# Kernel optimization log

Measured on AMD Instinct MI355X. Metric: run time of the kernel, lower is better.

The kernel has to match this reference:

```python
import jax, jax.numpy as jnp
import numpy as np

N = 100000   # nodes
E = 3200000  # edges (avg degree 32)
IN = 128     # in_channels
H = 128      # hidden_channels
G = 512      # graphs in batch


def setup_inputs() -> dict:
    key = jax.random.key(0)
    ks = jax.random.split(key, 8)
    x = jax.random.normal(ks[0], (N, IN), dtype=jnp.float32)
    edge_index = jax.random.randint(ks[1], (2, E), 0, N, dtype=jnp.int64)
    batch = jnp.sort(jax.random.randint(ks[2], (N,), 0, G, dtype=jnp.int64))
    s_in = 1.0 / np.sqrt(IN)
    s_h = 1.0 / np.sqrt(H)
    W1 = jax.random.normal(ks[3], (IN, H), dtype=jnp.float32) * s_in
    b1 = jnp.zeros((H,), dtype=jnp.float32)
    W2 = jax.random.normal(ks[4], (H, H), dtype=jnp.float32) * s_h
    b2 = jnp.zeros((H,), dtype=jnp.float32)
    Wc = jax.random.normal(ks[5], (H, 1), dtype=jnp.float32) * s_h
    bc = jnp.zeros((1,), dtype=jnp.float32)
    return {"x": x, "edge_index": edge_index, "batch": batch,
            "W1": W1, "b1": b1, "W2": W2, "b2": b2, "Wc": Wc, "bc": bc}


def _gcn_conv(x, W, b, src, dst, n):
    # PyG GCNConv: x' = D^{-1/2} (A+I) D^{-1/2} X W + b  (self-loops already in src/dst)
    h = x @ W                                      # [n, H] small GEMM
    ones = jnp.ones(src.shape[0], dtype=h.dtype)
    deg = jax.ops.segment_sum(ones, dst, num_segments=n)
    dinv = jnp.where(deg > 0, jax.lax.rsqrt(deg), 0.0)
    norm = dinv[src] * dinv[dst]                   # [E+n]
    msgs = h[src] * norm[:, None]                  # gather + scale (memory-bound)
    return jax.ops.segment_sum(msgs, dst, num_segments=n) + b


def reference(x, edge_index, batch, W1, b1, W2, b2, Wc, bc):
    n = x.shape[0]
    loop = jnp.arange(n, dtype=edge_index.dtype)
    src = jnp.concatenate([edge_index[0], loop])   # add self-loops
    dst = jnp.concatenate([edge_index[1], loop])
    h = jax.nn.relu(_gcn_conv(x, W1, b1, src, dst, n))
    h = jax.nn.relu(_gcn_conv(h, W2, b2, src, dst, n))
    # global_mean_pool: segment mean over graph ids
    counts = jax.ops.segment_sum(jnp.ones(n, dtype=h.dtype), batch, num_segments=G)
    sums = jax.ops.segment_sum(h, batch, num_segments=G)
    pooled = sums / jnp.maximum(counts, 1.0)[:, None]   # [G, H]
    return jax.nn.sigmoid(pooled @ Wc + bc)             # [G, 1]
```

## Files before the change

### kernel.cpp

```cpp
#include <hip/hip_runtime.h>

typedef unsigned short ushort_t;
typedef unsigned int uint_t;
typedef unsigned char u8_t;

typedef __bf16 bf16x8 __attribute__((ext_vector_type(8)));
typedef float f32x4 __attribute__((ext_vector_type(4)));
typedef uint_t uint32x4 __attribute__((ext_vector_type(4)));
typedef uint_t uint32x2 __attribute__((ext_vector_type(2)));
typedef _Float16 h2 __attribute__((ext_vector_type(2)));

#define EPB 16384
#define NSH 7
#define CAP 6144

__device__ __forceinline__ float b2f(ushort_t u) {
    union { uint_t ui; float f; } c; c.ui = ((uint_t)u) << 16; return c.f;
}
__device__ __forceinline__ ushort_t f2b(float f) {
    union { float f; uint_t ui; } c; c.f = f;
    uint_t u = c.ui;
    uint_t r = (u + 0x7fffu + ((u >> 16) & 1u)) >> 16;
    return (ushort_t)r;
}
__device__ __forceinline__ u8_t f2e5(float x) {
    ushort_t h = __builtin_bit_cast(ushort_t, (_Float16)x);
    uint_t r = ((uint_t)h + 0x7Fu + ((h >> 8) & 1u)) >> 8;
    return (u8_t)r;
}
__device__ __forceinline__ void upk_add(uint_t d, h2* acc) {
    uint_t A = __builtin_amdgcn_perm(0u, d, 0x010C000Cu);
    uint_t B = __builtin_amdgcn_perm(0u, d, 0x030C020Cu);
    acc[0] += __builtin_bit_cast(h2, A);
    acc[1] += __builtin_bit_cast(h2, B);
}

__global__ __launch_bounds__(256) void p1_hist(const int* __restrict__ dst,
                                               int* __restrict__ H,
                                               const float* __restrict__ W1,
                                               const float* __restrict__ W2,
                                               ushort_t* __restrict__ W1t,
                                               ushort_t* __restrict__ W2t,
                                               int E, int NBLK, int B) {
    int t = threadIdx.x, c = blockIdx.x;
    if (c >= NBLK) {
        int idx = (c - NBLK) * 256 + t;
        int sel = idx >> 14;
        int i = idx & 16383;
        int k = i >> 7, nn = i & 127;
        const float* S = sel ? W2 : W1;
        ushort_t* D = sel ? W2t : W1t;
        D[nn * 128 + k] = f2b(S[k * 128 + nn]);
        return;
    }
    __shared__ int hist[1024];
    for (int b = t; b < 1024; b += 256) hist[b] = 0;
    __syncthreads();
    int base = c * EPB;
    int lim = min(E - base, EPB);
    for (int i = t; i < lim; i += 256)
        atomicAdd(&hist[dst[base + i] >> NSH], 1);
    __syncthreads();
    for (int b = t; b < B; b += 256) H[b * NBLK + c] = hist[b];
}

__global__ __launch_bounds__(256) void reduce256(const int* __restrict__ in,
                                                 int* __restrict__ bsums, int n) {
    __shared__ int s[256];
    int t = threadIdx.x, g = blockIdx.x * 256 + t;
    s[t] = (g < n) ? in[g] : 0;
    __syncthreads();
    for (int o = 128; o > 0; o >>= 1) {
        if (t < o) s[t] += s[t + o];
        __syncthreads();
    }
    if (t == 0) bsums[blockIdx.x] = s[0];
}

__global__ __launch_bounds__(512) void scan_small(const int* __restrict__ in,
                                                  int* __restrict__ outEx, int n) {
    __shared__ int s[512];
    int t = threadIdx.x;
    int v = (t < n) ? in[t] : 0;
    s[t] = v;
    __syncthreads();
    for (int o = 1; o < 512; o <<= 1) {
        int x = 0;
        if (t >= o) x = s[t - o];
        __syncthreads();
        s[t] += x;
        __syncthreads();
    }
    if (t < n) outEx[t] = s[t] - v;
}

__global__ __launch_bounds__(256) void scan256ex(const int* __restrict__ in,
                                                 const int* __restrict__ boffs,
                                                 int* __restrict__ outEx, int n) {
    __shared__ int s[256];
    int t = threadIdx.x, g = blockIdx.x * 256 + t;
    int v = (g < n) ? in[g] : 0;
    s[t] = v;
    __syncthreads();
    for (int o = 1; o < 256; o <<= 1) {
        int x = 0;
        if (t >= o) x = s[t - o];
        __syncthreads();
        s[t] += x;
        __syncthreads();
    }
    if (g < n) outEx[g] = boffs[blockIdx.x] + s[t] - v;
}

__global__ __launch_bounds__(256) void p3_scatter(const int* __restrict__ src,
                                                  const int* __restrict__ dst,
                                                  const int* __restrict__ Hex,
                                                  uint_t* __restrict__ packed,
                                                  int E, int NBLK, int B) {
    __shared__ int offsL[1024];
    __shared__ int cur[1024];
    int t = threadIdx.x, c = blockIdx.x;
    for (int b = t; b < B; b += 256) {
        offsL[b] = Hex[b * NBLK + c];
        cur[b] = 0;
    }
    __syncthreads();
    int base = c * EPB;
    int lim = min(E - base, EPB);
    for (int i = t; i < lim; i += 256) {
        int d = dst[base + i];
        int s = src[base + i];
        int b = d >> NSH;
        int r = atomicAdd(&cur[b], 1);
        packed[offsL[b] + r] = ((uint_t)s << NSH) | (uint_t)(d & 127);
    }
}

__global__ __launch_bounds__(256) void p4_sort(const uint_t* __restrict__ packed,
                                               const int* __restrict__ Hex,
                                               uint_t* __restrict__ sorted,
                                               int E, int NBLK, int B) {
    __shared__ int hist[1024];
    __shared__ int hbase[1024];
    __shared__ int psum[256];
    int t = threadIdx.x, b = blockIdx.x;
    int bs = Hex[b * NBLK];
    int be = (b + 1 < B) ? Hex[(b + 1) * NBLK] : E;
    int m = be - bs;
    for (int i = t; i < 1024; i += 256) hist[i] = 0;
    __syncthreads();
    for (int i = t; i < m; i += 256)
        atomicAdd(&hist[packed[bs + i] >> (2 * NSH)], 1);
    __syncthreads();
    int v0 = hist[4 * t], v1 = hist[4 * t + 1], v2 = hist[4 * t + 2], v3 = hist[4 * t + 3];
    int tot = v0 + v1 + v2 + v3;
    psum[t] = tot;
    __syncthreads();
    for (int o = 1; o < 256; o <<= 1) {
        int x = 0;
        if (t >= o) x = psum[t - o];
        __syncthreads();
        psum[t] += x;
        __syncthreads();
    }
    int base = psum[t] - tot;
    hbase[4 * t]     = base;
    hbase[4 * t + 1] = base + v0;
    hbase[4 * t + 2] = base + v0 + v1;
    hbase[4 * t + 3] = base + v0 + v1 + v2;
    __syncthreads();
    for (int i = t; i < m; i += 256) {
        uint_t p = packed[bs + i];
        int k = p >> (2 * NSH);
        int r = atomicAdd(&hbase[k], 1);
        sorted[bs + r] = p;
    }
}

__global__ __launch_bounds__(256) void p4_csr(const uint_t* __restrict__ sorted,
                                              const int* __restrict__ Hex,
                                              int* __restrict__ adj,
                                              int* __restrict__ offs,
                                              float* __restrict__ dinv,
                                              int E, int N, int NBLK, int B) {
    __shared__ int cnt[128], loc[128], cur[128];
    __shared__ uint_t ebuf[CAP];
    int t = threadIdx.x, b = blockIdx.x;
    int bs = Hex[b * NBLK];
    int be = (b + 1 < B) ? Hex[(b + 1) * NBLK] : E;
    if (t < 128) cnt[t] = 0;
    __syncthreads();
    int m = be - bs;
    for (int i = t; i < m; i += 256) {
        uint_t p = sorted[bs + i];
        if (i < CAP) ebuf[i] = p;
        atomicAdd(&cnt[p & 127], 1);
    }
    __syncthreads();
    if (t < 128) loc[t] = cnt[t];
    __syncthreads();
    for (int o = 1; o < 128; o <<= 1) {
        int x = 0;
        if (t < 128 && t >= o) x = loc[t - o];
        __syncthreads();
        if (t < 128) loc[t] += x;
        __syncthreads();
    }
    if (t < 128) {
        int ex = loc[t] - cnt[t];
        int node = b * 128 + t;
        if (node < N) {
            offs[node] = bs + ex;
            dinv[node] = rsqrtf((float)(cnt[t] + 1));
        }
        loc[t] = ex;
        cur[t] = 0;
    }
    if (b == B - 1 && t == 0) offs[N] = E;
    __syncthreads();
    for (int i = t; i < m; i += 256) {
        uint_t p = (i < CAP) ? ebuf[i] : sorted[bs + i];
        int l = p & 127;
        int r = atomicAdd(&cur[l], 1);
        adj[bs + loc[l] + r] = (int)(p >> NSH);
    }
}

__global__ __launch_bounds__(256, 4) void gemm_scale(const ushort_t* __restrict__ Xin,
                                                     const ushort_t* __restrict__ Wt,
                                                     const float* __restrict__ dinv,
                                                     u8_t* __restrict__ Hout8, int n) {
    __shared__ ushort_t lds[128 * 136];
    int tid = threadIdx.x;
    for (int i = tid; i < 128 * 16; i += 256) {
        int r = i >> 4, c8 = (i & 15) << 3;
        *(uint32x4*)(lds + r * 136 + c8) = *(const uint32x4*)(Wt + r * 128 + c8);
    }
    __syncthreads();
    int lane = tid & 63, wave = tid >> 6;
    int m = lane & 15, q = lane >> 4;
    int row0 = blockIdx.x * 64 + wave * 16;
    int ar = row0 + m;
    if (ar > n - 1) ar = n - 1;
    bf16x8 a[4];
#pragma unroll
    for (int ks = 0; ks < 4; ++ks)
        a[ks] = __builtin_bit_cast(bf16x8,
            *(const uint32x4*)(Xin + (size_t)ar * 128 + ks * 32 + q * 8));
    f32x4 acc[8];
    f32x4 zero = {0.f, 0.f, 0.f, 0.f};
#pragma unroll
    for (int nt = 0; nt < 8; ++nt) acc[nt] = zero;
#pragma unroll
    for (int nt = 0; nt < 8; ++nt) {
#pragma unroll
        for (int ks = 0; ks < 4; ++ks) {
            bf16x8 b = __builtin_bit_cast(bf16x8,
                *(const uint32x4*)(lds + (nt * 16 + m) * 136 + ks * 32 + q * 8));
            acc[nt] = __builtin_amdgcn_mfma_f32_16x16x32_bf16(a[ks], b, acc[nt], 0, 0, 0);
        }
    }
    float dv[4];
#pragma unroll
    for (int r = 0; r < 4; ++r) {
        int gr = row0 + q * 4 + r;
        dv[r] = (gr < n) ? dinv[gr] : 0.f;
    }
#pragma unroll
    for (int nt = 0; nt < 8; ++nt) {
#pragma unroll
        for (int r = 0; r < 4; ++r) {
            int gr = row0 + q * 4 + r;
            if (gr < n)
                Hout8[(size_t)gr * 128 + nt * 16 + m] = f2e5(acc[nt][r] * dv[r]);
        }
    }
}

__global__ __launch_bounds__(256, 4) void gemm_scale_f32(const float* __restrict__ Xf,
                                                         const ushort_t* __restrict__ Wt,
                                                         const float* __restrict__ dinv,
                                                         u8_t* __restrict__ Hout8, int n) {
    __shared__ ushort_t lds[128 * 136];
    int tid = threadIdx.x;
    for (int i = tid; i < 128 * 16; i += 256) {
        int r = i >> 4, c8 = (i & 15) << 3;
        *(uint32x4*)(lds + r * 136 + c8) = *(const uint32x4*)(Wt + r * 128 + c8);
    }
    __syncthreads();
    int lane = tid & 63, wave = tid >> 6;
    int m = lane & 15, q = lane >> 4;
    int row0 = blockIdx.x * 64 + wave * 16;
    int ar = row0 + m;
    if (ar > n - 1) ar = n - 1;
    bf16x8 a[4];
#pragma unroll
    for (int ks = 0; ks < 4; ++ks) {
        const float* p = Xf + (size_t)ar * 128 + ks * 32 + q * 8;
        f32x4 lo = *(const f32x4*)p;
        f32x4 hi = *(const f32x4*)(p + 4);
        ushort_t t[8];
        t[0] = f2b(lo[0]); t[1] = f2b(lo[1]); t[2] = f2b(lo[2]); t[3] = f2b(lo[3]);
        t[4] = f2b(hi[0]); t[5] = f2b(hi[1]); t[6] = f2b(hi[2]); t[7] = f2b(hi[3]);
        a[ks] = __builtin_bit_cast(bf16x8, *(uint32x4*)t);
    }
    f32x4 acc[8];
    f32x4 zero = {0.f, 0.f, 0.f, 0.f};
#pragma unroll
    for (int nt = 0; nt < 8; ++nt) acc[nt] = zero;
#pragma unroll
    for (int nt = 0; nt < 8; ++nt) {
#pragma unroll
        for (int ks = 0; ks < 4; ++ks) {
            bf16x8 b = __builtin_bit_cast(bf16x8,
                *(const uint32x4*)(lds + (nt * 16 + m) * 136 + ks * 32 + q * 8));
            acc[nt] = __builtin_amdgcn_mfma_f32_16x16x32_bf16(a[ks], b, acc[nt], 0, 0, 0);
        }
    }
    float dv[4];
#pragma unroll
    for (int r = 0; r < 4; ++r) {
        int gr = row0 + q * 4 + r;
        dv[r] = (gr < n) ? dinv[gr] : 0.f;
    }
#pragma unroll
    for (int nt = 0; nt < 8; ++nt) {
#pragma unroll
        for (int r = 0; r < 4; ++r) {
            int gr = row0 + q * 4 + r;
            if (gr < n)
                Hout8[(size_t)gr * 128 + nt * 16 + m] = f2e5(acc[nt][r] * dv[r]);
        }
    }
}

__global__ __launch_bounds__(256, 8) void agg_kernel(const u8_t* __restrict__ Hs8,
                                                     const int* __restrict__ adj,
                                                     const int* __restrict__ offs,
                                                     const float* __restrict__ dinv,
                                                     const float* __restrict__ bias,
                                                     ushort_t* __restrict__ Out, int n) {
    int node = blockIdx.x * 4 + (threadIdx.x >> 6);
    if (node >= n) return;
    int lane = threadIdx.x & 63;
    int g = lane >> 4;
    int l16 = lane & 15;
    int col = l16 * 8;
    const u8_t* base8 = Hs8 + col;
    const int beg = offs[node], end = offs[node + 1];
    h2 acc[4];
    h2 hz = {(_Float16)0.f, (_Float16)0.f};
#pragma unroll
    for (int k = 0; k < 4; ++k) acc[k] = hz;
    if (g == 0) {
        uint32x2 w = *(const uint32x2*)(base8 + (size_t)node * 128);
        upk_add(w[0], acc);
        upk_add(w[1], acc + 2);
    }
    int e = beg;
    for (; e + 16 <= end; e += 16) {
        int s0 = adj[e + g];
        int s1 = adj[e + 4 + g];
        int s2 = adj[e + 8 + g];
        int s3 = adj[e + 12 + g];
        uint32x2 w0 = *(const uint32x2*)(base8 + (size_t)s0 * 128);
        uint32x2 w1 = *(const uint32x2*)(base8 + (size_t)s1 * 128);
        uint32x2 w2 = *(const uint32x2*)(base8 + (size_t)s2 * 128);
        uint32x2 w3 = *(const uint32x2*)(base8 + (size_t)s3 * 128);
        upk_add(w0[0], acc); upk_add(w0[1], acc + 2);
        upk_add(w1[0], acc); upk_add(w1[1], acc + 2);
        upk_add(w2[0], acc); upk_add(w2[1], acc + 2);
        upk_add(w3[0], acc); upk_add(w3[1], acc + 2);
    }
    for (; e < end; e += 4) {
        int idx = e + g;
        if (idx < end) {
            int s = adj[idx];
            uint32x2 w = *(const uint32x2*)(base8 + (size_t)s * 128);
            upk_add(w[0], acc);
            upk_add(w[1], acc + 2);
        }
    }
#pragma unroll
    for (int k = 0; k < 4; ++k) {
        uint_t v = __builtin_bit_cast(uint_t, acc[k]);
        acc[k] += __builtin_bit_cast(h2, (uint_t)__shfl_xor(v, 16, 64));
        v = __builtin_bit_cast(uint_t, acc[k]);
        acc[k] += __builtin_bit_cast(h2, (uint_t)__shfl_xor(v, 32, 64));
    }
    if (g == 0) {
        float di = dinv[node];
        ushort_t o[8];
#pragma unroll
        for (int k = 0; k < 4; ++k) {
            float f0 = (float)acc[k][0];
            float f1 = (float)acc[k][1];
            o[2 * k]     = f2b(fmaxf(di * f0 + bias[col + 2 * k], 0.f));
            o[2 * k + 1] = f2b(fmaxf(di * f1 + bias[col + 2 * k + 1], 0.f));
        }
        *(uint32x4*)(Out + (size_t)node * 128 + col) = *(uint32x4*)o;
    }
}

__global__ __launch_bounds__(256, 8) void agg_pool_kernel(const u8_t* __restrict__ Hs8,
                                                          const int* __restrict__ adj,
                                                          const int* __restrict__ offs,
                                                          const float* __restrict__ dinv,
                                                          const float* __restrict__ bias,
                                                          const float* __restrict__ Wc,
                                                          float* __restrict__ Sout, int n) {
    int node = blockIdx.x * 4 + (threadIdx.x >> 6);
    if (node >= n) return;
    int lane = threadIdx.x & 63;
    int g = lane >> 4;
    int l16 = lane & 15;
    int col = l16 * 8;
    const u8_t* base8 = Hs8 + col;
    const int beg = offs[node], end = offs[node + 1];
    h2 acc[4];
    h2 hz = {(_Float16)0.f, (_Float16)0.f};
#pragma unroll
    for (int k = 0; k < 4; ++k) acc[k] = hz;
    if (g == 0) {
        uint32x2 w = *(const uint32x2*)(base8 + (size_t)node * 128);
        upk_add(w[0], acc);
        upk_add(w[1], acc + 2);
    }
    int e = beg;
    for (; e + 16 <= end; e += 16) {
        int s0 = adj[e + g];
        int s1 = adj[e + 4 + g];
        int s2 = adj[e + 8 + g];
        int s3 = adj[e + 12 + g];
        uint32x2 w0 = *(const uint32x2*)(base8 + (size_t)s0 * 128);
        uint32x2 w1 = *(const uint32x2*)(base8 + (size_t)s1 * 128);
        uint32x2 w2 = *(const uint32x2*)(base8 + (size_t)s2 * 128);
        uint32x2 w3 = *(const uint32x2*)(base8 + (size_t)s3 * 128);
        upk_add(w0[0], acc); upk_add(w0[1], acc + 2);
        upk_add(w1[0], acc); upk_add(w1[1], acc + 2);
        upk_add(w2[0], acc); upk_add(w2[1], acc + 2);
        upk_add(w3[0], acc); upk_add(w3[1], acc + 2);
    }
    for (; e < end; e += 4) {
        int idx = e + g;
        if (idx < end) {
            int s = adj[idx];
            uint32x2 w = *(const uint32x2*)(base8 + (size_t)s * 128);
            upk_add(w[0], acc);
            upk_add(w[1], acc + 2);
        }
    }
#pragma unroll
    for (int k = 0; k < 4; ++k) {
        uint_t v = __builtin_bit_cast(uint_t, acc[k]);
        acc[k] += __builtin_bit_cast(h2, (uint_t)__shfl_xor(v, 16, 64));
        v = __builtin_bit_cast(uint_t, acc[k]);
        acc[k] += __builtin_bit_cast(h2, (uint_t)__shfl_xor(v, 32, 64));
    }
    float local = 0.f;
    float di = dinv[node];
#pragma unroll
    for (int k = 0; k < 4; ++k) {
        float f0 = fmaxf(di * (float)acc[k][0] + bias[col + 2 * k], 0.f);
        float f1 = fmaxf(di * (float)acc[k][1] + bias[col + 2 * k + 1], 0.f);
        local += f0 * Wc[col + 2 * k] + f1 * Wc[col + 2 * k + 1];
    }
    local += __shfl_xor(local, 1, 64);
    local += __shfl_xor(local, 2, 64);
    local += __shfl_xor(local, 4, 64);
    local += __shfl_xor(local, 8, 64);
    if (lane == 0) Sout[node] = local;
}

__global__ __launch_bounds__(256) void pool2_kernel(const float* __restrict__ S,
                                                    const int* __restrict__ batch,
                                                    const float* __restrict__ bc,
                                                    float* __restrict__ out, int n) {
    int g = blockIdx.x;
    int t = threadIdx.x;
    int lo = 0, hi = n;
    while (lo < hi) { int mid = (lo + hi) >> 1; if (batch[mid] < g) lo = mid + 1; else hi = mid; }
    int start = lo;
    hi = n;
    while (lo < hi) { int mid = (lo + hi) >> 1; if (batch[mid] < g + 1) lo = mid + 1; else hi = mid; }
    int stop = lo;
    float s = 0.f;
    for (int i = start + t; i < stop; i += 256) s += S[i];
    __shared__ float red[256];
    red[t] = s;
    __syncthreads();
    for (int o = 128; o > 0; o >>= 1) {
        if (t < o) red[t] += red[t + o];
        __syncthreads();
    }
    if (t == 0) {
        int cg = stop - start;
        float z = red[0] / (float)(cg > 0 ? cg : 1) + bc[0];
        out[g] = 1.f / (1.f + expf(-z));
    }
}

extern "C" void kernel_launch(void* const* d_in, const int* in_sizes, int n_in,
                              void* d_out, int out_size, void* d_ws, size_t ws_size,
                              hipStream_t stream) {
    const float* X     = (const float*)d_in[0];
    const int* ei      = (const int*)d_in[1];
    const int* batch   = (const int*)d_in[2];
    const float* W1    = (const float*)d_in[3];
    const float* b1    = (const float*)d_in[4];
    const float* W2    = (const float*)d_in[5];
    const float* b2    = (const float*)d_in[6];
    const float* Wc    = (const float*)d_in[7];
    const float* bc    = (const float*)d_in[8];

    const int N = in_sizes[2];
    const int E = in_sizes[1] / 2;
    const int G = out_size;
    const int* srcv = ei;
    const int* dstv = ei + E;

    const int NBLK = (E + EPB - 1) / EPB;
    const int B    = (N + 127) >> NSH;
    const int n0   = B * NBLK;
    const int g1   = (n0 + 255) / 256;
    const int g2   = (g1 + 255) / 256;

    char* p = (char*)d_ws;
    auto alloc = [&](size_t bytes) -> void* {
        void* r = (void*)p;
        p += (bytes + 255) & ~(size_t)255;
        return r;
    };
    int* H         = (int*)alloc((size_t)n0 * 4);
    int* Hex       = (int*)alloc((size_t)n0 * 4);
    int* S1        = (int*)alloc((size_t)g1 * 4);
    int* S1ex      = (int*)alloc((size_t)g1 * 4);
    int* S2        = (int*)alloc((size_t)g2 * 4);
    int* S2ex      = (int*)alloc((size_t)g2 * 4);
    uint_t* packed = (uint_t*)alloc((size_t)E * 4);
    uint_t* sorted = (uint_t*)alloc((size_t)E * 4);
    int* adj       = (int*)packed;
    int* offs      = (int*)alloc(((size_t)N + 1) * 4);
    float* dinv    = (float*)alloc((size_t)N * 4);
    ushort_t* W1t  = (ushort_t*)alloc(16384 * 2);
    ushort_t* W2t  = (ushort_t*)alloc(16384 * 2);
    u8_t* h8       = (u8_t*)alloc((size_t)N * 128);
    ushort_t* bufA = (ushort_t*)alloc((size_t)N * 128 * 2);
    float* Snode   = (float*)alloc((size_t)N * 4);

    p1_hist<<<NBLK + 128, 256, 0, stream>>>(dstv, H, W1, W2, W1t, W2t, E, NBLK, B);
    reduce256<<<g1, 256, 0, stream>>>(H, S1, n0);
    reduce256<<<g2, 256, 0, stream>>>(S1, S2, g1);
    scan_small<<<1, 512, 0, stream>>>(S2, S2ex, g2);
    scan256ex<<<g2, 256, 0, stream>>>(S1, S2ex, S1ex, g1);
    scan256ex<<<g1, 256, 0, stream>>>(H, S1ex, Hex, n0);
    p3_scatter<<<NBLK, 256, 0, stream>>>(srcv, dstv, Hex, packed, E, NBLK, B);
    p4_sort<<<B, 256, 0, stream>>>(packed, Hex, sorted, E, NBLK, B);
    p4_csr<<<B, 256, 0, stream>>>(sorted, Hex, adj, offs, dinv, E, N, NBLK, B);

    const int GB = (N + 63) / 64;
    const int AB = (N + 3) / 4;
    gemm_scale_f32<<<GB, 256, 0, stream>>>(X, W1t, dinv, h8, N);
    agg_kernel<<<AB, 256, 0, stream>>>(h8, adj, offs, dinv, b1, bufA, N);
    gemm_scale<<<GB, 256, 0, stream>>>(bufA, W2t, dinv, h8, N);
    agg_pool_kernel<<<AB, 256, 0, stream>>>(h8, adj, offs, dinv, b2, Wc, Snode, N);
    pool2_kernel<<<G, 256, 0, stream>>>(Snode, batch, bc, (float*)d_out, N);
}
```

Measured before the change: 410.7 us.

## Fuse bucket sort and CSR build in LDS, shorten scan chain, unroll gather

Merges the p4_sort and p4_csr kernels into one p4_build kernel. It keeps each 128-node bucket's edges in shared memory, sorts them there by source high bits and writes the adjacency directly, which drops one global round trip over all edges and one launch. EPB grows so there are fewer edge blocks, which lets the prefix scan skip one reduce/scan level and uses two fewer launches. The aggregation gather loop is unrolled to 8 outstanding neighbor loads per lane for more memory-level parallelism. The cost is higher LDS use per block and more registers in the aggregation kernels, plus a fallback path when a bucket exceeds CAP that skips the source sort.

```diff
diff --git a/kernel.cpp b/kernel.cpp
--- a/kernel.cpp
+++ b/kernel.cpp
@@ -10,7 +10,7 @@
 typedef uint_t uint32x2 __attribute__((ext_vector_type(2)));
 typedef _Float16 h2 __attribute__((ext_vector_type(2)));
 
-#define EPB 16384
+#define EPB 20480
 #define NSH 7
 #define CAP 6144
 
@@ -136,21 +136,32 @@
     }
 }
 
-__global__ __launch_bounds__(256) void p4_sort(const uint_t* __restrict__ packed,
-                                               const int* __restrict__ Hex,
-                                               uint_t* __restrict__ sorted,
-                                               int E, int NBLK, int B) {
+__global__ __launch_bounds__(256) void p4_build(const uint_t* __restrict__ packed,
+                                                const int* __restrict__ Hex,
+                                                int* __restrict__ adj,
+                                                int* __restrict__ offs,
+                                                float* __restrict__ dinv,
+                                                int E, int N, int NBLK, int B) {
+    __shared__ uint_t ebuf[CAP];
+    __shared__ uint_t sbuf[CAP];
     __shared__ int hist[1024];
     __shared__ int hbase[1024];
     __shared__ int psum[256];
+    __shared__ int dcnt[128], loc[128], cur[128];
     int t = threadIdx.x, b = blockIdx.x;
     int bs = Hex[b * NBLK];
     int be = (b + 1 < B) ? Hex[(b + 1) * NBLK] : E;
     int m = be - bs;
     for (int i = t; i < 1024; i += 256) hist[i] = 0;
-    __syncthreads();
-    for (int i = t; i < m; i += 256)
-        atomicAdd(&hist[packed[bs + i] >> (2 * NSH)], 1);
+    if (t < 128) dcnt[t] = 0;
+    __syncthreads();
+    bool fits = (m <= CAP);
+    for (int i = t; i < m; i += 256) {
+        uint_t p = packed[bs + i];
+        if (fits) ebuf[i] = p;
+        atomicAdd(&dcnt[p & 127], 1);
+        atomicAdd(&hist[p >> (2 * NSH)], 1);
+    }
     __syncthreads();
     int v0 = hist[4 * t], v1 = hist[4 * t + 1], v2 = hist[4 * t + 2], v3 = hist[4 * t + 3];
     int tot = v0 + v1 + v2 + v3;
@@ -168,36 +179,7 @@
     hbase[4 * t + 1] = base + v0;
     hbase[4 * t + 2] = base + v0 + v1;
     hbase[4 * t + 3] = base + v0 + v1 + v2;
-    __syncthreads();
-    for (int i = t; i < m; i += 256) {
-        uint_t p = packed[bs + i];
-        int k = p >> (2 * NSH);
-        int r = atomicAdd(&hbase[k], 1);
-        sorted[bs + r] = p;
-    }
-}
-
-__global__ __launch_bounds__(256) void p4_csr(const uint_t* __restrict__ sorted,
-                                              const int* __restrict__ Hex,
-                                              int* __restrict__ adj,
-                                              int* __restrict__ offs,
-                                              float* __restrict__ dinv,
-                                              int E, int N, int NBLK, int B) {
-    __shared__ int cnt[128], loc[128], cur[128];
-    __shared__ uint_t ebuf[CAP];
-    int t = threadIdx.x, b = blockIdx.x;
-    int bs = Hex[b * NBLK];
-    int be = (b + 1 < B) ? Hex[(b + 1) * NBLK] : E;
-    if (t < 128) cnt[t] = 0;
-    __syncthreads();
-    int m = be - bs;
-    for (int i = t; i < m; i += 256) {
-        uint_t p = sorted[bs + i];
-        if (i < CAP) ebuf[i] = p;
-        atomicAdd(&cnt[p & 127], 1);
-    }
-    __syncthreads();
-    if (t < 128) loc[t] = cnt[t];
+    if (t < 128) loc[t] = dcnt[t];
     __syncthreads();
     for (int o = 1; o < 128; o <<= 1) {
         int x = 0;
@@ -207,22 +189,37 @@
         __syncthreads();
     }
     if (t < 128) {
-        int ex = loc[t] - cnt[t];
+        int ex = loc[t] - dcnt[t];
         int node = b * 128 + t;
         if (node < N) {
             offs[node] = bs + ex;
-            dinv[node] = rsqrtf((float)(cnt[t] + 1));
+            dinv[node] = rsqrtf((float)(dcnt[t] + 1));
         }
         loc[t] = ex;
         cur[t] = 0;
     }
     if (b == B - 1 && t == 0) offs[N] = E;
     __syncthreads();
-    for (int i = t; i < m; i += 256) {
-        uint_t p = (i < CAP) ? ebuf[i] : sorted[bs + i];
-        int l = p & 127;
-        int r = atomicAdd(&cur[l], 1);
-        adj[bs + loc[l] + r] = (int)(p >> NSH);
+    if (fits) {
+        for (int i = t; i < m; i += 256) {
+            uint_t p = ebuf[i];
+            int r = atomicAdd(&hbase[p >> (2 * NSH)], 1);
+            sbuf[r] = p;
+        }
+        __syncthreads();
+        for (int i = t; i < m; i += 256) {
+            uint_t p = sbuf[i];
+            int l = p & 127;
+            int r = atomicAdd(&cur[l], 1);
+            adj[bs + loc[l] + r] = (int)(p >> NSH);
+        }
+    } else {
+        for (int i = t; i < m; i += 256) {
+            uint_t p = packed[bs + i];
+            int l = p & 127;
+            int r = atomicAdd(&cur[l], 1);
+            adj[bs + loc[l] + r] = (int)(p >> NSH);
+        }
     }
 }
 
@@ -330,6 +327,40 @@
             int gr = row0 + q * 4 + r;
             if (gr < n)
                 Hout8[(size_t)gr * 128 + nt * 16 + m] = f2e5(acc[nt][r] * dv[r]);
+        }
+    }
+}
+
+__device__ __forceinline__ void agg_body(const u8_t* base8, const int* __restrict__ adj,
+                                         int beg, int end, int g, h2* acc) {
+    int e = beg;
+    for (; e + 32 <= end; e += 32) {
+        int s[8];
+#pragma unroll
+        for (int j = 0; j < 8; ++j) s[j] = adj[e + 4 * j + g];
+        uint32x2 w[8];
+#pragma unroll
+        for (int j = 0; j < 8; ++j) w[j] = *(const uint32x2*)(base8 + (size_t)s[j] * 128);
+#pragma unroll
+        for (int j = 0; j < 8; ++j) {
+            upk_add(w[j][0], acc);
+            upk_add(w[j][1], acc + 2);
+        }
+    }
+    for (; e + 8 <= end; e += 8) {
+        int s0 = adj[e + g], s1 = adj[e + 4 + g];
+        uint32x2 w0 = *(const uint32x2*)(base8 + (size_t)s0 * 128);
+        uint32x2 w1 = *(const uint32x2*)(base8 + (size_t)s1 * 128);
+        upk_add(w0[0], acc); upk_add(w0[1], acc + 2);
+        upk_add(w1[0], acc); upk_add(w1[1], acc + 2);
+    }
+    for (; e < end; e += 4) {
+        int idx = e + g;
+        if (idx < end) {
+            int s = adj[idx];
+            uint32x2 w = *(const uint32x2*)(base8 + (size_t)s * 128);
+            upk_add(w[0], acc);
+            upk_add(w[1], acc + 2);
         }
     }
 }
@@ -357,30 +388,7 @@
         upk_add(w[0], acc);
         upk_add(w[1], acc + 2);
     }
-    int e = beg;
-    for (; e + 16 <= end; e += 16) {
-        int s0 = adj[e + g];
-        int s1 = adj[e + 4 + g];
-        int s2 = adj[e + 8 + g];
-        int s3 = adj[e + 12 + g];
-        uint32x2 w0 = *(const uint32x2*)(base8 + (size_t)s0 * 128);
-        uint32x2 w1 = *(const uint32x2*)(base8 + (size_t)s1 * 128);
-        uint32x2 w2 = *(const uint32x2*)(base8 + (size_t)s2 * 128);
-        uint32x2 w3 = *(const uint32x2*)(base8 + (size_t)s3 * 128);
-        upk_add(w0[0], acc); upk_add(w0[1], acc + 2);
-        upk_add(w1[0], acc); upk_add(w1[1], acc + 2);
-        upk_add(w2[0], acc); upk_add(w2[1], acc + 2);
-        upk_add(w3[0], acc); upk_add(w3[1], acc + 2);
-    }
-    for (; e < end; e += 4) {
-        int idx = e + g;
-        if (idx < end) {
-            int s = adj[idx];
-            uint32x2 w = *(const uint32x2*)(base8 + (size_t)s * 128);
-            upk_add(w[0], acc);
-            upk_add(w[1], acc + 2);
-        }
-    }
+    agg_body(base8, adj, beg, end, g, acc);
 #pragma unroll
     for (int k = 0; k < 4; ++k) {
         uint_t v = __builtin_bit_cast(uint_t, acc[k]);
@@ -426,30 +434,7 @@
         upk_add(w[0], acc);
         upk_add(w[1], acc + 2);
     }
-    int e = beg;
-    for (; e + 16 <= end; e += 16) {
-        int s0 = adj[e + g];
-        int s1 = adj[e + 4 + g];
-        int s2 = adj[e + 8 + g];
-        int s3 = adj[e + 12 + g];
-        uint32x2 w0 = *(const uint32x2*)(base8 + (size_t)s0 * 128);
-        uint32x2 w1 = *(const uint32x2*)(base8 + (size_t)s1 * 128);
-        uint32x2 w2 = *(const uint32x2*)(base8 + (size_t)s2 * 128);
-        uint32x2 w3 = *(const uint32x2*)(base8 + (size_t)s3 * 128);
-        upk_add(w0[0], acc); upk_add(w0[1], acc + 2);
-        upk_add(w1[0], acc); upk_add(w1[1], acc + 2);
-        upk_add(w2[0], acc); upk_add(w2[1], acc + 2);
-        upk_add(w3[0], acc); upk_add(w3[1], acc + 2);
-    }
-    for (; e < end; e += 4) {
-        int idx = e + g;
-        if (idx < end) {
-            int s = adj[idx];
-            uint32x2 w = *(const uint32x2*)(base8 + (size_t)s * 128);
-            upk_add(w[0], acc);
-            upk_add(w[1], acc + 2);
-        }
-    }
+    agg_body(base8, adj, beg, end, g, acc);
 #pragma unroll
     for (int k = 0; k < 4; ++k) {
         uint_t v = __builtin_bit_cast(uint_t, acc[k]);
@@ -523,7 +508,6 @@
     const int B    = (N + 127) >> NSH;
     const int n0   = B * NBLK;
     const int g1   = (n0 + 255) / 256;
-    const int g2   = (g1 + 255) / 256;
 
     char* p = (char*)d_ws;
     auto alloc = [&](size_t bytes) -> void* {
@@ -535,11 +519,8 @@
     int* Hex       = (int*)alloc((size_t)n0 * 4);
     int* S1        = (int*)alloc((size_t)g1 * 4);
     int* S1ex      = (int*)alloc((size_t)g1 * 4);
-    int* S2        = (int*)alloc((size_t)g2 * 4);
-    int* S2ex      = (int*)alloc((size_t)g2 * 4);
     uint_t* packed = (uint_t*)alloc((size_t)E * 4);
-    uint_t* sorted = (uint_t*)alloc((size_t)E * 4);
-    int* adj       = (int*)packed;
+    int* adj       = (int*)alloc((size_t)E * 4);
     int* offs      = (int*)alloc(((size_t)N + 1) * 4);
     float* dinv    = (float*)alloc((size_t)N * 4);
     ushort_t* W1t  = (ushort_t*)alloc(16384 * 2);
@@ -550,13 +531,10 @@
 
     p1_hist<<<NBLK + 128, 256, 0, stream>>>(dstv, H, W1, W2, W1t, W2t, E, NBLK, B);
     reduce256<<<g1, 256, 0, stream>>>(H, S1, n0);
-    reduce256<<<g2, 256, 0, stream>>>(S1, S2, g1);
-    scan_small<<<1, 512, 0, stream>>>(S2, S2ex, g2);
-    scan256ex<<<g2, 256, 0, stream>>>(S1, S2ex, S1ex, g1);
+    scan_small<<<1, 512, 0, stream>>>(S1, S1ex, g1);
     scan256ex<<<g1, 256, 0, stream>>>(H, S1ex, Hex, n0);
     p3_scatter<<<NBLK, 256, 0, stream>>>(srcv, dstv, Hex, packed, E, NBLK, B);
-    p4_sort<<<B, 256, 0, stream>>>(packed, Hex, sorted, E, NBLK, B);
-    p4_csr<<<B, 256, 0, stream>>>(sorted, Hex, adj, offs, dinv, E, N, NBLK, B);
+    p4_build<<<B, 256, 0, stream>>>(packed, Hex, adj, offs, dinv, E, N, NBLK, B);
 
     const int GB = (N + 63) / 64;
     const int AB = (N + 3) / 4;
```

Result: faster. 398.3 us (-3.0%).
